# Kernel optimization log

Measured on AMD Instinct MI355X. Metric: run time of the kernel, lower is better.

The kernel has to match this reference:

```python
import jax, jax.numpy as jnp
import numpy as np

B, N, W, D = 32, 576, 32, 256  # batch, patches, max concepts per sample, embed dim


def _l2norm(x, eps=1e-12):
    # matches torch F.normalize: x / max(||x||, eps)
    n = jnp.linalg.norm(x, axis=-1, keepdims=True)
    return x / jnp.maximum(n, eps)


def setup_inputs() -> dict:
    key = jax.random.key(0)
    k1, k2, k3 = jax.random.split(key, 3)
    return {
        "image_token_features": jax.random.normal(k1, (B, N, D), dtype=jnp.float32),
        "concept_text_features": jax.random.normal(k2, (B, W, D), dtype=jnp.float32),
        "concept_lengths": jax.random.randint(k3, (B,), 1, W + 1, dtype=jnp.int32),
        "logit_scale": jnp.array([2.0], dtype=jnp.float32),   # log-scale, clamp(-10,10).exp()
        "logit_bias": jnp.array([-1.0], dtype=jnp.float32),
    }


def reference(image_token_features, concept_text_features, logit_scale, logit_bias, concept_lengths):
    img = _l2norm(image_token_features)          # (B, N, D)
    con = _l2norm(concept_text_features)         # (B, W, D)
    # A[m, c, n, w] = cos(patch_n of image m, concept_w of sample c)
    A = jnp.einsum('mnd,cwd->mcnw', img, con)    # (B, B, N, W) -- dominant intermediate
    max_per_concept = A.max(axis=2)              # max over patches -> (B, B, W)
    # masked mean over valid concepts (ragged lengths)
    mask = (jnp.arange(W)[None, :] < concept_lengths[:, None]).astype(img.dtype)  # (B, W)
    lens = concept_lengths.astype(img.dtype)     # all >= 1 by construction
    sim = jnp.sum(max_per_concept * mask[None, :, :], axis=-1) / lens[None, :]    # (B, B)
    t = jnp.exp(jnp.clip(logit_scale, -10.0, 10.0))[0]
    logits = jnp.clip(t * sim + logit_bias[0], -50.0, 50.0)
    z = 2.0 * jnp.eye(sim.shape[0], dtype=sim.dtype) - 1.0  # +1 diag, -1 off-diag
    loss = -jnp.mean(jax.nn.log_sigmoid(z * logits))
    return loss
```

## Files before the change

### kernel.cpp

```cpp
#include <hip/hip_runtime.h>
#include <hip/hip_bf16.h>
#include <math.h>

#define BB 32
#define NP 576
#define WW 32
#define DD 256

typedef __bf16 bf16x8 __attribute__((ext_vector_type(8)));
typedef float f32x4 __attribute__((ext_vector_type(4)));

__device__ __forceinline__ unsigned short f2bf(float f) {
  unsigned int u = __float_as_uint(f);
  u += 0x7FFFu + ((u >> 16) & 1u);
  return (unsigned short)(u >> 16);
}

__global__ __launch_bounds__(256) void norm_cast_kernel(
    const float* __restrict__ img, const float* __restrict__ con,
    unsigned short* __restrict__ img_bf, unsigned short* __restrict__ con_bf) {
  int row = blockIdx.x * 4 + (threadIdx.x >> 6);
  int lane = threadIdx.x & 63;
  const int n_img = BB * NP;
  const float* src;
  unsigned short* dst;
  if (row < n_img) {
    src = img + (size_t)row * DD;
    dst = img_bf + (size_t)row * DD;
  } else {
    int r2 = row - n_img;
    src = con + (size_t)r2 * DD;
    dst = con_bf + (size_t)r2 * DD;
  }
  float4 v = ((const float4*)src)[lane];
  float ss = v.x * v.x + v.y * v.y + v.z * v.z + v.w * v.w;
  #pragma unroll
  for (int off = 1; off < 64; off <<= 1) ss += __shfl_xor(ss, off);
  float inv = 1.0f / fmaxf(sqrtf(ss), 1e-12f);
  ushort4 o;
  o.x = f2bf(v.x * inv);
  o.y = f2bf(v.y * inv);
  o.z = f2bf(v.z * inv);
  o.w = f2bf(v.w * inv);
  ((ushort4*)dst)[lane] = o;
}

__global__ __launch_bounds__(256, 3) void gemm_max_kernel(
    const unsigned short* __restrict__ img_bf,
    const unsigned short* __restrict__ con_bf,
    float* __restrict__ P) {
  int bx = blockIdx.x;
  int bw = bx & 7;
  int bm = bx >> 3;
  int R0 = bm * 128;
  int w0 = bw * 128;

  __shared__ __align__(16) unsigned char lds[33 * 1024];
  unsigned char* ldsA = lds;
  unsigned char* ldsB = lds + 16384;
  float* sm = (float*)(lds + 32768);

  int tid = threadIdx.x;
  int wid = tid >> 6;
  int lane = tid & 63;
  int q = lane >> 4;
  int r = lane & 15;
  int wp = wid >> 1;
  int wc = wid & 1;

  f32x4 acc[4][4];
  #pragma unroll
  for (int i = 0; i < 4; ++i)
    #pragma unroll
    for (int j = 0; j < 4; ++j) acc[i][j] = (f32x4){0.f, 0.f, 0.f, 0.f};

  for (int kb = 0; kb < 4; ++kb) {
    __syncthreads();
    #pragma unroll
    for (int j = 0; j < 4; ++j) {
      int g = j * 256 + wid * 64 + lane;
      int row = g >> 3;
      int sl = (g & 7) ^ (row & 7);
      const unsigned short* ga = img_bf + (size_t)(R0 + row) * DD + kb * 64 + sl * 8;
      const unsigned short* gb = con_bf + (size_t)(w0 + row) * DD + kb * 64 + sl * 8;
      unsigned char* la = ldsA + (j * 256 + wid * 64) * 16;
      unsigned char* lb = ldsB + (j * 256 + wid * 64) * 16;
      __builtin_amdgcn_global_load_lds(
          (const __attribute__((address_space(1))) unsigned int*)ga,
          (__attribute__((address_space(3))) unsigned int*)la, 16, 0, 0);
      __builtin_amdgcn_global_load_lds(
          (const __attribute__((address_space(1))) unsigned int*)gb,
          (__attribute__((address_space(3))) unsigned int*)lb, 16, 0, 0);
    }
    __syncthreads();
    #pragma unroll
    for (int kk = 0; kk < 2; ++kk) {
      bf16x8 af[4], bfr[4];
      int sw = ((((kk << 2) | q) ^ (r & 7)) << 4);
      #pragma unroll
      for (int pi = 0; pi < 4; ++pi) {
        int arow = wp * 64 + pi * 16 + r;
        af[pi] = *(const bf16x8*)(ldsA + arow * 128 + sw);
      }
      #pragma unroll
      for (int wj = 0; wj < 4; ++wj) {
        int brow = wc * 64 + wj * 16 + r;
        bfr[wj] = *(const bf16x8*)(ldsB + brow * 128 + sw);
      }
      #pragma unroll
      for (int pi = 0; pi < 4; ++pi)
        #pragma unroll
        for (int wj = 0; wj < 4; ++wj)
          acc[pi][wj] =
              __builtin_amdgcn_mfma_f32_16x16x32_bf16(af[pi], bfr[wj], acc[pi][wj], 0, 0, 0);
    }
  }

  float mxw[4];
  #pragma unroll
  for (int wj = 0; wj < 4; ++wj) {
    float v = -1e30f;
    #pragma unroll
    for (int pi = 0; pi < 4; ++pi) {
      v = fmaxf(v, fmaxf(fmaxf(acc[pi][wj][0], acc[pi][wj][1]),
                         fmaxf(acc[pi][wj][2], acc[pi][wj][3])));
    }
    v = fmaxf(v, __shfl_xor(v, 16));
    v = fmaxf(v, __shfl_xor(v, 32));
    mxw[wj] = v;
  }
  __syncthreads();
  if (lane < 16) {
    #pragma unroll
    for (int wj = 0; wj < 4; ++wj)
      sm[wp * 128 + wc * 64 + wj * 16 + lane] = mxw[wj];
  }
  __syncthreads();
  if (tid < 128) {
    int i0 = (2 * bm) / 9;
    int slot = bm - (9 * i0) / 2;
    bool crossing = ((2 * bm) % 9) == 8;
    float vlo = sm[tid];
    float vhi = sm[128 + tid];
    if (crossing) {
      P[(size_t)(i0 * 5 + slot) * 1024 + w0 + tid] = vlo;
      P[(size_t)((i0 + 1) * 5) * 1024 + w0 + tid] = vhi;
    } else {
      P[(size_t)(i0 * 5 + slot) * 1024 + w0 + tid] = fmaxf(vlo, vhi);
    }
  }
}

__global__ __launch_bounds__(256) void reduce_kernel(
    const float* __restrict__ P, const int* __restrict__ lengths,
    float* __restrict__ sims) {
  int pair = blockIdx.x * 4 + (threadIdx.x >> 6);
  int lane = threadIdx.x & 63;
  int m = pair >> 5;
  int c = pair & 31;
  int w = lane & 31;
  const float* base = P + (size_t)(m * 5) * 1024 + c * 32 + w;
  float v = base[0];
  v = fmaxf(v, base[1024]);
  v = fmaxf(v, base[2048]);
  v = fmaxf(v, base[3072]);
  v = fmaxf(v, base[4096]);
  int len = lengths[c];
  float contrib = (w < len) ? v : 0.0f;
  #pragma unroll
  for (int off = 1; off < 32; off <<= 1) contrib += __shfl_xor(contrib, off);
  if (lane == 0) sims[pair] = contrib / (float)len;
}

__global__ __launch_bounds__(256) void loss_kernel(
    const float* __restrict__ sims, const float* __restrict__ lscale,
    const float* __restrict__ lbias, float* __restrict__ out) {
  float tt = expf(fminf(fmaxf(lscale[0], -10.0f), 10.0f));
  float bias = lbias[0];
  int tid = threadIdx.x;
  float acc = 0.0f;
  for (int p = tid; p < BB * BB; p += 256) {
    int mm = p >> 5;
    int cc = p & 31;
    float lg = fminf(fmaxf(tt * sims[p] + bias, -50.0f), 50.0f);
    float x = (mm == cc) ? lg : -lg;
    float ls = (x >= 0.0f) ? -log1pf(expf(-x)) : (x - log1pf(expf(x)));
    acc += ls;
  }
  #pragma unroll
  for (int off = 1; off < 64; off <<= 1) acc += __shfl_xor(acc, off);
  __shared__ float s[4];
  if ((tid & 63) == 0) s[tid >> 6] = acc;
  __syncthreads();
  if (tid == 0) out[0] = -(s[0] + s[1] + s[2] + s[3]) / (float)(BB * BB);
}

extern "C" void kernel_launch(void* const* d_in, const int* in_sizes, int n_in,
                              void* d_out, int out_size, void* d_ws, size_t ws_size,
                              hipStream_t stream) {
  const float* img = (const float*)d_in[0];
  const float* con = (const float*)d_in[1];
  const int* lens = (const int*)d_in[2];
  const float* lsc = (const float*)d_in[3];
  const float* lbi = (const float*)d_in[4];

  unsigned short* img_bf = (unsigned short*)d_ws;
  unsigned short* con_bf = img_bf + (size_t)BB * NP * DD;
  float* P = (float*)(con_bf + (size_t)BB * WW * DD);
  float* sims = P + (size_t)160 * 1024;

  norm_cast_kernel<<<(BB * NP + BB * WW) / 4, 256, 0, stream>>>(img, con, img_bf, con_bf);
  gemm_max_kernel<<<144 * 8, 256, 0, stream>>>(img_bf, con_bf, P);
  reduce_kernel<<<256, 256, 0, stream>>>(P, lens, sims);
  loss_kernel<<<1, 256, 0, stream>>>(sims, lsc, lbi, (float*)d_out);
}
```

Measured before the change: 95.10 us.

## Enlarge GEMM M-tile to 192 rows and fuse reduce with loss kernel

Each GEMM block now covers 192 image rows, so a 576-patch image splits into exactly three tiles and the boundary-crossing partial-max logic goes away. That leaves 768 blocks instead of 1152, each with more MFMA work per B-tile load, at the cost of more accumulator registers and more LDS. The reduce and loss kernels are merged with a last-block-done atomic counter, which is reset inside the normalization kernel, so one kernel launch is removed.

```diff
diff --git a/kernel.cpp b/kernel.cpp
--- a/kernel.cpp
+++ b/kernel.cpp
@@ -18,7 +18,9 @@
 
 __global__ __launch_bounds__(256) void norm_cast_kernel(
     const float* __restrict__ img, const float* __restrict__ con,
-    unsigned short* __restrict__ img_bf, unsigned short* __restrict__ con_bf) {
+    unsigned short* __restrict__ img_bf, unsigned short* __restrict__ con_bf,
+    int* __restrict__ cnt) {
+  if (blockIdx.x == 0 && threadIdx.x == 0) *cnt = 0;
   int row = blockIdx.x * 4 + (threadIdx.x >> 6);
   int lane = threadIdx.x & 63;
   const int n_img = BB * NP;
@@ -52,13 +54,13 @@
   int bx = blockIdx.x;
   int bw = bx & 7;
   int bm = bx >> 3;
-  int R0 = bm * 128;
+  int R0 = bm * 192;
   int w0 = bw * 128;
 
-  __shared__ __align__(16) unsigned char lds[33 * 1024];
+  __shared__ __align__(16) unsigned char lds[41984];
   unsigned char* ldsA = lds;
-  unsigned char* ldsB = lds + 16384;
-  float* sm = (float*)(lds + 32768);
+  unsigned char* ldsB = lds + 24576;
+  float* sm = (float*)(lds + 40960);
 
   int tid = threadIdx.x;
   int wid = tid >> 6;
@@ -68,26 +70,32 @@
   int wp = wid >> 1;
   int wc = wid & 1;
 
-  f32x4 acc[4][4];
-  #pragma unroll
-  for (int i = 0; i < 4; ++i)
+  f32x4 acc[6][4];
+  #pragma unroll
+  for (int i = 0; i < 6; ++i)
     #pragma unroll
     for (int j = 0; j < 4; ++j) acc[i][j] = (f32x4){0.f, 0.f, 0.f, 0.f};
 
   for (int kb = 0; kb < 4; ++kb) {
     __syncthreads();
+    #pragma unroll
+    for (int j = 0; j < 6; ++j) {
+      int g = j * 256 + wid * 64 + lane;
+      int row = g >> 3;
+      int sl = (g & 7) ^ (row & 7);
+      const unsigned short* ga = img_bf + (size_t)(R0 + row) * DD + kb * 64 + sl * 8;
+      unsigned char* la = ldsA + (j * 256 + wid * 64) * 16;
+      __builtin_amdgcn_global_load_lds(
+          (const __attribute__((address_space(1))) unsigned int*)ga,
+          (__attribute__((address_space(3))) unsigned int*)la, 16, 0, 0);
+    }
     #pragma unroll
     for (int j = 0; j < 4; ++j) {
       int g = j * 256 + wid * 64 + lane;
       int row = g >> 3;
       int sl = (g & 7) ^ (row & 7);
-      const unsigned short* ga = img_bf + (size_t)(R0 + row) * DD + kb * 64 + sl * 8;
       const unsigned short* gb = con_bf + (size_t)(w0 + row) * DD + kb * 64 + sl * 8;
-      unsigned char* la = ldsA + (j * 256 + wid * 64) * 16;
       unsigned char* lb = ldsB + (j * 256 + wid * 64) * 16;
-      __builtin_amdgcn_global_load_lds(
-          (const __attribute__((address_space(1))) unsigned int*)ga,
-          (__attribute__((address_space(3))) unsigned int*)la, 16, 0, 0);
       __builtin_amdgcn_global_load_lds(
           (const __attribute__((address_space(1))) unsigned int*)gb,
           (__attribute__((address_space(3))) unsigned int*)lb, 16, 0, 0);
@@ -95,24 +103,22 @@
     __syncthreads();
     #pragma unroll
     for (int kk = 0; kk < 2; ++kk) {
-      bf16x8 af[4], bfr[4];
       int sw = ((((kk << 2) | q) ^ (r & 7)) << 4);
-      #pragma unroll
-      for (int pi = 0; pi < 4; ++pi) {
-        int arow = wp * 64 + pi * 16 + r;
-        af[pi] = *(const bf16x8*)(ldsA + arow * 128 + sw);
-      }
+      bf16x8 bfr[4];
       #pragma unroll
       for (int wj = 0; wj < 4; ++wj) {
         int brow = wc * 64 + wj * 16 + r;
         bfr[wj] = *(const bf16x8*)(ldsB + brow * 128 + sw);
       }
       #pragma unroll
-      for (int pi = 0; pi < 4; ++pi)
+      for (int pi = 0; pi < 6; ++pi) {
+        int arow = wp * 96 + pi * 16 + r;
+        bf16x8 af = *(const bf16x8*)(ldsA + arow * 128 + sw);
         #pragma unroll
         for (int wj = 0; wj < 4; ++wj)
           acc[pi][wj] =
-              __builtin_amdgcn_mfma_f32_16x16x32_bf16(af[pi], bfr[wj], acc[pi][wj], 0, 0, 0);
+              __builtin_amdgcn_mfma_f32_16x16x32_bf16(af, bfr[wj], acc[pi][wj], 0, 0, 0);
+      }
     }
   }
 
@@ -121,7 +127,7 @@
   for (int wj = 0; wj < 4; ++wj) {
     float v = -1e30f;
     #pragma unroll
-    for (int pi = 0; pi < 4; ++pi) {
+    for (int pi = 0; pi < 6; ++pi) {
       v = fmaxf(v, fmaxf(fmaxf(acc[pi][wj][0], acc[pi][wj][1]),
                          fmaxf(acc[pi][wj][2], acc[pi][wj][3])));
     }
@@ -137,47 +143,39 @@
   }
   __syncthreads();
   if (tid < 128) {
-    int i0 = (2 * bm) / 9;
-    int slot = bm - (9 * i0) / 2;
-    bool crossing = ((2 * bm) % 9) == 8;
-    float vlo = sm[tid];
-    float vhi = sm[128 + tid];
-    if (crossing) {
-      P[(size_t)(i0 * 5 + slot) * 1024 + w0 + tid] = vlo;
-      P[(size_t)((i0 + 1) * 5) * 1024 + w0 + tid] = vhi;
-    } else {
-      P[(size_t)(i0 * 5 + slot) * 1024 + w0 + tid] = fmaxf(vlo, vhi);
-    }
-  }
-}
-
-__global__ __launch_bounds__(256) void reduce_kernel(
+    float v = fmaxf(sm[tid], sm[128 + tid]);
+    P[(size_t)bm * 1024 + w0 + tid] = v;
+  }
+}
+
+__global__ __launch_bounds__(256) void reduce_loss_kernel(
     const float* __restrict__ P, const int* __restrict__ lengths,
-    float* __restrict__ sims) {
-  int pair = blockIdx.x * 4 + (threadIdx.x >> 6);
-  int lane = threadIdx.x & 63;
+    const float* __restrict__ lscale, const float* __restrict__ lbias,
+    float* __restrict__ sims, int* __restrict__ cnt, float* __restrict__ out) {
+  int tid = threadIdx.x;
+  int pair = blockIdx.x * 4 + (tid >> 6);
+  int lane = tid & 63;
   int m = pair >> 5;
   int c = pair & 31;
   int w = lane & 31;
-  const float* base = P + (size_t)(m * 5) * 1024 + c * 32 + w;
-  float v = base[0];
-  v = fmaxf(v, base[1024]);
-  v = fmaxf(v, base[2048]);
-  v = fmaxf(v, base[3072]);
-  v = fmaxf(v, base[4096]);
+  const float* base = P + (size_t)(m * 3) * 1024 + c * 32 + w;
+  float v = fmaxf(fmaxf(base[0], base[1024]), base[2048]);
   int len = lengths[c];
   float contrib = (w < len) ? v : 0.0f;
   #pragma unroll
   for (int off = 1; off < 32; off <<= 1) contrib += __shfl_xor(contrib, off);
   if (lane == 0) sims[pair] = contrib / (float)len;
-}
-
-__global__ __launch_bounds__(256) void loss_kernel(
-    const float* __restrict__ sims, const float* __restrict__ lscale,
-    const float* __restrict__ lbias, float* __restrict__ out) {
+
+  __threadfence();
+  __syncthreads();
+  __shared__ int lastflag;
+  if (tid == 0) lastflag = (atomicAdd(cnt, 1) == gridDim.x - 1) ? 1 : 0;
+  __syncthreads();
+  if (!lastflag) return;
+  __threadfence();
+
   float tt = expf(fminf(fmaxf(lscale[0], -10.0f), 10.0f));
   float bias = lbias[0];
-  int tid = threadIdx.x;
   float acc = 0.0f;
   for (int p = tid; p < BB * BB; p += 256) {
     int mm = p >> 5;
@@ -207,10 +205,10 @@
   unsigned short* img_bf = (unsigned short*)d_ws;
   unsigned short* con_bf = img_bf + (size_t)BB * NP * DD;
   float* P = (float*)(con_bf + (size_t)BB * WW * DD);
-  float* sims = P + (size_t)160 * 1024;
-
-  norm_cast_kernel<<<(BB * NP + BB * WW) / 4, 256, 0, stream>>>(img, con, img_bf, con_bf);
-  gemm_max_kernel<<<144 * 8, 256, 0, stream>>>(img_bf, con_bf, P);
-  reduce_kernel<<<256, 256, 0, stream>>>(P, lens, sims);
-  loss_kernel<<<1, 256, 0, stream>>>(sims, lsc, lbi, (float*)d_out);
-}
+  float* sims = P + (size_t)96 * 1024;
+  int* cnt = (int*)(sims + 1024);
+
+  norm_cast_kernel<<<(BB * NP + BB * WW) / 4, 256, 0, stream>>>(img, con, img_bf, con_bf, cnt);
+  gemm_max_kernel<<<96 * 8, 256, 0, stream>>>(img_bf, con_bf, P);
+  reduce_loss_kernel<<<256, 256, 0, stream>>>(P, lens, lsc, lbi, sims, cnt, (float*)d_out);
+}
```

New measurement: 111.8 us. 1.18x slower.
